# Kernel optimization log

Hardware: AMD Instinct MI355X
Metric: run time of the kernel (lower is better)

Reference implementation:

```python
import jax, jax.numpy as jnp
import numpy as np

B, S, HID = 1, 2048, 2048
H, KVH, D, VD = 32, 8, 128, 128
R = 64  # rope_dim = head_dim * partial_rotary_factor, rounded down to even
N_REP = H // KVH
SCALE = D ** -0.5
NEG = -1e9


def _rotate_half(x):
    half = x.shape[-1] // 2
    return jnp.concatenate([-x[..., half:], x[..., :half]], axis=-1)


def setup_inputs() -> dict:
    key = jax.random.key(0)
    ks = jax.random.split(key, 8)
    hidden_states = jax.random.normal(ks[0], (B, S, HID), dtype=jnp.float32)
    # RoPE angles: standard inverse-frequency positional embedding of width R
    inv_freq = 1.0 / (10000.0 ** (np.arange(0, R, 2, dtype=np.float32) / R))
    pos = np.arange(S, dtype=np.float32)
    freqs = np.outer(pos, inv_freq)                       # [S, R/2]
    emb = np.concatenate([freqs, freqs], axis=-1)         # [S, R]
    cos = jnp.asarray(np.cos(emb))[None].repeat(B, axis=0)  # [B, S, R]
    sin = jnp.asarray(np.sin(emb))[None].repeat(B, axis=0)
    # additive causal mask [B, 1, S, S]
    causal = jnp.triu(jnp.full((S, S), NEG, dtype=jnp.float32), k=1)
    attention_mask = jnp.broadcast_to(causal[None, None], (B, 1, S, S))
    std = 0.02
    Wq = jax.random.normal(ks[1], (H * D, HID), dtype=jnp.float32) * std
    Wk = jax.random.normal(ks[2], (KVH * D, HID), dtype=jnp.float32) * std
    Wv = jax.random.normal(ks[3], (KVH * VD, HID), dtype=jnp.float32) * std
    Wo = jax.random.normal(ks[4], (HID, H * VD), dtype=jnp.float32) * std
    sink_bias = jax.random.normal(ks[5], (H,), dtype=jnp.float32) * 0.5
    return {"hidden_states": hidden_states, "cos": cos, "sin": sin,
            "attention_mask": attention_mask, "Wq": Wq, "Wk": Wk, "Wv": Wv,
            "Wo": Wo, "sink_bias": sink_bias}


def reference(hidden_states, cos, sin, attention_mask, Wq, Wk, Wv, Wo, sink_bias):
    b, s, _ = hidden_states.shape
    # projections -> [B, heads, S, dim]
    q = (hidden_states @ Wq.T).reshape(b, s, H, D).transpose(0, 2, 1, 3)
    k = (hidden_states @ Wk.T).reshape(b, s, KVH, D).transpose(0, 2, 1, 3)
    v = (hidden_states @ Wv.T).reshape(b, s, KVH, VD).transpose(0, 2, 1, 3)
    # partial RoPE on first R dims
    c = cos[:, None, :, :]  # [B,1,S,R]
    si = sin[:, None, :, :]
    q_r, q_n = q[..., :R], q[..., R:]
    k_r, k_n = k[..., :R], k[..., R:]
    q = jnp.concatenate([q_r * c + _rotate_half(q_r) * si, q_n], axis=-1)
    k = jnp.concatenate([k_r * c + _rotate_half(k_r) * si, k_n], axis=-1)
    # GQA: repeat kv heads
    k_rep = jnp.repeat(k, N_REP, axis=1)
    v_rep = jnp.repeat(v, N_REP, axis=1)
    scores = jnp.einsum('bhqd,bhkd->bhqk', q, k_rep) * SCALE + attention_mask
    # extra attention-sink logit column per head
    sinks = jnp.broadcast_to(sink_bias.reshape(1, H, 1, 1), (b, H, s, 1))
    aw = jnp.concatenate([scores, sinks], axis=-1)            # [B,H,S,S+1]
    probs = jax.nn.softmax(aw, axis=-1)[..., :-1]             # drop sink column
    out = jnp.einsum('bhqk,bhkd->bhqd', probs, v_rep)
    out = out.transpose(0, 2, 1, 3).reshape(b, s, H * VD)
    return out @ Wo.T
```

## Files before the change

kernel.cpp:

```cpp
#include <hip/hip_runtime.h>

typedef unsigned short u16;
typedef unsigned int   u32;
typedef __bf16  bf16x8 __attribute__((ext_vector_type(8)));
typedef float   f32x4  __attribute__((ext_vector_type(4)));
typedef u16     u16x4  __attribute__((ext_vector_type(4)));
typedef u16     u16x8  __attribute__((ext_vector_type(8)));

#define S_LEN 2048
#define NH 32
#define NKVH 8
#define HD 128
#define QKVST 6144
#define AOST  4096
#define ATT_SCALE 0.08838834764831845f
#define RESCALE_THR 8.0f

__device__ __forceinline__ u16 f2bf(float f){
  u32 u = __builtin_bit_cast(u32, f);
  u += 0x7FFFu + ((u >> 16) & 1u);
  return (u16)(u >> 16);
}
__device__ __forceinline__ float bf2f(u16 h){
  u32 u = ((u32)h) << 16;
  return __builtin_bit_cast(float, u);
}
__device__ __forceinline__ void gload_lds16(const u16* g, u16* l){
  __builtin_amdgcn_global_load_lds(
      (const __attribute__((address_space(1))) void*)g,
      (__attribute__((address_space(3))) void*)l, 16, 0, 0);
}

__global__ void cvt_kernel(const f32x4* __restrict__ in, u16x4* __restrict__ out, int n4){
  int i = blockIdx.x * 256 + threadIdx.x;
  if (i >= n4) return;
  f32x4 v = in[i];
  u16x4 o;
  o[0] = f2bf(v[0]); o[1] = f2bf(v[1]); o[2] = f2bf(v[2]); o[3] = f2bf(v[3]);
  out[i] = o;
}

template<int OUT_BF16, int ROPE>
__global__ __launch_bounds__(256, 2)
void gemm_bt_kernel(const u16* __restrict__ X, const u16* __restrict__ W,
                    void* __restrict__ Cv, int M, int N, int K,
                    const float* __restrict__ cosv, const float* __restrict__ sinv){
  __shared__ __align__(16) u16 As[2][2][128 * 32];
  __shared__ __align__(16) u16 Bs[2][2][128 * 32];
  const int m0 = blockIdx.y * 128, n0 = blockIdx.x * 128;
  const int tid = threadIdx.x;
  const int wave = tid >> 6, lane = tid & 63;
  const int wm = wave >> 1, wn = wave & 1;
  const int g = lane >> 4, ln = lane & 15;
  const int r0 = tid >> 2;
  const int cc = (tid & 3) * 8;
  f32x4 acc[4][4] = {};
  const u16* xa0 = X + (size_t)(m0 + r0) * K + cc;
  const u16* xa1 = X + (size_t)(m0 + r0 + 64) * K + cc;
  const u16* wb0 = W + (size_t)(n0 + r0) * K + cc;
  const u16* wb1 = W + (size_t)(n0 + r0 + 64) * K + cc;

  auto stage = [&](int buf, int k0){
    #pragma unroll
    for (int s = 0; s < 2; s++){
      const int kc = k0 + s * 32;
      gload_lds16(xa0 + kc, &As[buf][s][tid * 8]);
      gload_lds16(xa1 + kc, &As[buf][s][2048 + tid * 8]);
      gload_lds16(wb0 + kc, &Bs[buf][s][tid * 8]);
      gload_lds16(wb1 + kc, &Bs[buf][s][2048 + tid * 8]);
    }
  };

  stage(0, 0);
  __syncthreads();
  int cur = 0;
  for (int k0 = 0; k0 < K; k0 += 64){
    if (k0 + 64 < K) stage(cur ^ 1, k0 + 64);
    #pragma unroll
    for (int s = 0; s < 2; s++){
      bf16x8 a[4], b[4];
      #pragma unroll
      for (int f = 0; f < 4; f++) a[f] = *(const bf16x8*)&As[cur][s][(wm * 64 + f * 16 + ln) * 32 + g * 8];
      #pragma unroll
      for (int f = 0; f < 4; f++) b[f] = *(const bf16x8*)&Bs[cur][s][(wn * 64 + f * 16 + ln) * 32 + g * 8];
      __builtin_amdgcn_s_setprio(1);
      #pragma unroll
      for (int i = 0; i < 4; i++)
        #pragma unroll
        for (int j = 0; j < 4; j++)
          acc[i][j] = __builtin_amdgcn_mfma_f32_16x16x32_bf16(a[i], b[j], acc[i][j], 0, 0, 0);
      __builtin_amdgcn_s_setprio(0);
    }
    __syncthreads();
    cur ^= 1;
  }
  if (ROPE && wn == 0 && n0 < 5120){
    #pragma unroll
    for (int i = 0; i < 4; i++)
      #pragma unroll
      for (int r = 0; r < 4; r++){
        const int row = m0 + wm * 64 + i * 16 + g * 4 + r;
        #pragma unroll
        for (int j = 0; j < 2; j++){
          const int d = j * 16 + ln;
          float c  = cosv[row * 64 + d];
          float sn = sinv[row * 64 + d];
          float x0 = acc[i][j][r], x1 = acc[i][j + 2][r];
          acc[i][j][r]     = x0 * c - x1 * sn;
          acc[i][j + 2][r] = x1 * c + x0 * sn;
        }
      }
  }
  #pragma unroll
  for (int i = 0; i < 4; i++)
    #pragma unroll
    for (int j = 0; j < 4; j++)
      #pragma unroll
      for (int r = 0; r < 4; r++){
        int row = m0 + wm * 64 + i * 16 + g * 4 + r;
        int col = n0 + wn * 64 + j * 16 + ln;
        if (OUT_BF16) ((u16*)Cv)[(size_t)row * N + col] = f2bf(acc[i][j][r]);
        else          ((float*)Cv)[(size_t)row * N + col] = acc[i][j][r];
      }
}

__global__ void vtrans_kernel(const u16* __restrict__ QKV, u16* __restrict__ VT){
  int idx = blockIdx.x * 256 + threadIdx.x;
  if (idx >= NKVH * HD * S_LEN) return;
  int s   = idx & (S_LEN - 1);
  int vd  = (idx >> 11) & (HD - 1);
  int kvh = idx >> 18;
  VT[idx] = QKV[(size_t)s * QKVST + 5120 + kvh * HD + vd];
}

__global__ __launch_bounds__(256, 2)
void attn_kernel(const u16* __restrict__ QKV, const u16* __restrict__ VT,
                 const float* __restrict__ sinkb, u16* __restrict__ AO){
  __shared__ __align__(16) u16 Ks[2][64 * 128];
  __shared__ __align__(16) u16 Vs[2][144 * 64];
  __shared__ __align__(16) u16 Ps[4][16 * 64];
  const int b   = blockIdx.x;
  const int kvh = b & 7;
  const int h   = kvh * 4 + ((b >> 3) & 3);
  const int qt  = 31 - (b >> 5);
  const int tid = threadIdx.x;
  const int w = tid >> 6, lane = tid & 63;
  const int g = lane >> 4, ln = lane & 15;
  const int q0 = qt * 64;
  const int qw = q0 + w * 16;

  const u16* Kbase = QKV + 4096 + kvh * HD;
  const u16* Vbase = VT + (size_t)kvh * HD * S_LEN;

  auto stage = [&](int buf, int kt){
    const int k0 = kt * 64;
    #pragma unroll
    for (int p = 0; p < 4; p++){
      int idx = p * 256 + tid;
      int r = idx >> 4, c16 = idx & 15;
      gload_lds16(Kbase + (size_t)(k0 + r) * QKVST + ((c16 ^ (r & 7)) * 8), &Ks[buf][idx * 8]);
    }
    #pragma unroll
    for (int p = 0; p < 4; p++){
      int idx = p * 256 + tid;
      int vd = idx >> 3, c8 = idx & 7;
      gload_lds16(Vbase + (size_t)vd * S_LEN + k0 + ((c8 ^ (vd & 7)) * 8), &Vs[buf][idx * 8]);
    }
  };

  for (int i = tid; i < 16 * 64; i += 256){
    u16 v = (i < 64) ? (u16)0x3F80 : (u16)0;
    Vs[0][128 * 64 + i] = v;
    Vs[1][128 * 64 + i] = v;
  }

  bf16x8 qf[4];
  const u16* qrow = QKV + (size_t)(qw + ln) * QKVST + h * HD;
  #pragma unroll
  for (int t = 0; t < 4; t++) qf[t] = *(const bf16x8*)(qrow + t * 32 + g * 8);

  f32x4 O[9] = {};
  float m_r[4];
  #pragma unroll
  for (int r = 0; r < 4; r++) m_r[r] = -3.0e38f;

  const int nkt = qt + 1;
  stage(0, 0);
  __syncthreads();
  int cur = 0;

  for (int kt = 0; kt < nkt; kt++){
    const int k0 = kt * 64;
    if (kt + 1 < nkt) stage(cur ^ 1, kt + 1);

    const u16* Kc = Ks[cur];
    f32x4 sc[4] = {};
    __builtin_amdgcn_s_setprio(1);
    #pragma unroll
    for (int f = 0; f < 4; f++){
      const int krow = f * 16 + ln;
      #pragma unroll
      for (int t = 0; t < 4; t++){
        bf16x8 kf = *(const bf16x8*)&Kc[krow * 128 + ((t * 32 + g * 8) ^ ((ln & 7) << 3))];
        sc[f] = __builtin_amdgcn_mfma_f32_16x16x32_bf16(qf[t], kf, sc[f], 0, 0, 0);
      }
    }
    __builtin_amdgcn_s_setprio(0);

    const bool diag = (kt == qt);
    float pv[4][4];
    #pragma unroll
    for (int f = 0; f < 4; f++)
      #pragma unroll
      for (int r = 0; r < 4; r++){
        float v = sc[f][r] * ATT_SCALE;
        if (diag && (k0 + f * 16 + ln > qw + g * 4 + r)) v = -1e30f;
        pv[f][r] = v;
      }
    float mx[4];
    #pragma unroll
    for (int r = 0; r < 4; r++){
      float t = fmaxf(fmaxf(pv[0][r], pv[1][r]), fmaxf(pv[2][r], pv[3][r]));
      #pragma unroll
      for (int d = 1; d < 16; d <<= 1) t = fmaxf(t, __shfl_xor(t, d));
      mx[r] = t;
    }
    int ok = (mx[0] <= m_r[0] + RESCALE_THR) & (mx[1] <= m_r[1] + RESCALE_THR)
           & (mx[2] <= m_r[2] + RESCALE_THR) & (mx[3] <= m_r[3] + RESCALE_THR);
    if (!__all(ok)){
      float sf_[4];
      #pragma unroll
      for (int r = 0; r < 4; r++){
        float mn = fmaxf(m_r[r], mx[r]);
        sf_[r] = __expf(m_r[r] - mn);
        m_r[r] = mn;
      }
      #pragma unroll
      for (int fn = 0; fn < 9; fn++)
        #pragma unroll
        for (int r = 0; r < 4; r++) O[fn][r] *= sf_[r];
    }
    u16* Pw = Ps[w];
    #pragma unroll
    for (int r = 0; r < 4; r++){
      const int row = g * 4 + r;
      #pragma unroll
      for (int f = 0; f < 4; f++){
        float p = __expf(pv[f][r] - m_r[r]);
        Pw[row * 64 + ((f * 16 + ln) ^ ((row & 7) << 3))] = f2bf(p);
      }
    }
    const u16* Vc = Vs[cur];
    bf16x8 pa0 = *(const bf16x8*)&Pw[ln * 64 + ((g * 8)      ^ ((ln & 7) << 3))];
    bf16x8 pa1 = *(const bf16x8*)&Pw[ln * 64 + ((32 + g * 8) ^ ((ln & 7) << 3))];
    __builtin_amdgcn_s_setprio(1);
    #pragma unroll
    for (int fn = 0; fn < 9; fn++){
      const int vr = fn * 16 + ln;
      bf16x8 v0 = *(const bf16x8*)&Vc[vr * 64 + ((g * 8)      ^ ((ln & 7) << 3))];
      bf16x8 v1 = *(const bf16x8*)&Vc[vr * 64 + ((32 + g * 8) ^ ((ln & 7) << 3))];
      O[fn] = __builtin_amdgcn_mfma_f32_16x16x32_bf16(pa0, v0, O[fn], 0, 0, 0);
      O[fn] = __builtin_amdgcn_mfma_f32_16x16x32_bf16(pa1, v1, O[fn], 0, 0, 0);
    }
    __builtin_amdgcn_s_setprio(0);

    __syncthreads();
    cur ^= 1;
  }
  float sb = sinkb[h];
  #pragma unroll
  for (int r = 0; r < 4; r++){
    float l = __shfl(O[8][r], lane & 48);
    float mt = fmaxf(m_r[r], sb);
    float lt = l * __expf(m_r[r] - mt) + __expf(sb - mt);
    float osc = __expf(m_r[r] - mt) / lt;
    #pragma unroll
    for (int fn = 0; fn < 8; fn++)
      AO[(size_t)(qw + g * 4 + r) * AOST + h * HD + fn * 16 + ln] = f2bf(O[fn][r] * osc);
  }
}

extern "C" void kernel_launch(void* const* d_in, const int* in_sizes, int n_in,
                              void* d_out, int out_size, void* d_ws, size_t ws_size,
                              hipStream_t stream){
  (void)in_sizes; (void)n_in; (void)out_size; (void)ws_size;
  const float* hs    = (const float*)d_in[0];
  const float* cosv  = (const float*)d_in[1];
  const float* sinv  = (const float*)d_in[2];
  const float* Wq    = (const float*)d_in[4];
  const float* Wk    = (const float*)d_in[5];
  const float* Wv    = (const float*)d_in[6];
  const float* Wo    = (const float*)d_in[7];
  const float* sinkb = (const float*)d_in[8];
  float* out = (float*)d_out;

  char* ws = (char*)d_ws;
  u16* XB    = (u16*)(ws);
  u16* WQKVB = (u16*)(ws + 8388608);
  u16* WOB   = (u16*)(ws + 33554432);
  u16* QKV   = (u16*)(ws + 50331648);
  u16* VT    = (u16*)(ws + 75497472);
  u16* AO    = (u16*)(ws + 79691776);

  cvt_kernel<<<4096, 256, 0, stream>>>((const f32x4*)hs, (u16x4*)XB, 1048576);
  cvt_kernel<<<8192, 256, 0, stream>>>((const f32x4*)Wq, (u16x4*)WQKVB, 2097152);
  cvt_kernel<<<2048, 256, 0, stream>>>((const f32x4*)Wk, (u16x4*)(WQKVB + 4096 * 2048), 524288);
  cvt_kernel<<<2048, 256, 0, stream>>>((const f32x4*)Wv, (u16x4*)(WQKVB + 5120 * 2048), 524288);
  cvt_kernel<<<8192, 256, 0, stream>>>((const f32x4*)Wo, (u16x4*)WOB, 2097152);

  gemm_bt_kernel<1, 1><<<dim3(48, 16), 256, 0, stream>>>(XB, WQKVB, QKV, 2048, 6144, 2048, cosv, sinv);

  vtrans_kernel<<<8192, 256, 0, stream>>>(QKV, VT);

  attn_kernel<<<dim3(1024), 256, 0, stream>>>(QKV, VT, sinkb, AO);

  gemm_bt_kernel<0, 0><<<dim3(16, 16), 256, 0, stream>>>(AO, WOB, out, 2048, 2048, 4096, nullptr, nullptr);
}
```

Before: 259.3 us.

## Merge conversion launches, fold softmax scale into Q, skip masked diagonal tiles

The five fp32-to-bf16 conversion launches become one kernel, relying on the workspace buffers being laid out contiguously. The QKV GEMM epilogue pre-multiplies Q by scale*log2e so attention can use exp2 without a per-score multiply. The row sum now comes from a separate MFMA against a ones fragment instead of a padded ninth V tile, which shrinks V shared memory. On the causal diagonal, fully masked 16-column fragments are skipped in QK and set to zero in P. Together these cut launch overhead and some ALU and MFMA work. The trade-offs are Q being rounded to bf16 after scaling and extra branching inside the attention loop.

```diff
diff --git a/kernel.cpp b/kernel.cpp
--- a/kernel.cpp
+++ b/kernel.cpp
@@ -14,7 +14,9 @@
 #define QKVST 6144
 #define AOST  4096
 #define ATT_SCALE 0.08838834764831845f
-#define RESCALE_THR 8.0f
+#define LOG2E 1.4426950408889634f
+#define QSC2 (ATT_SCALE * LOG2E)
+#define RESCALE_THR2 11.5f
 
 __device__ __forceinline__ u16 f2bf(float f){
   u32 u = __builtin_bit_cast(u32, f);
@@ -31,10 +33,17 @@
       (__attribute__((address_space(3))) void*)l, 16, 0, 0);
 }
 
-__global__ void cvt_kernel(const f32x4* __restrict__ in, u16x4* __restrict__ out, int n4){
+__global__ void cvt_all_kernel(const f32x4* __restrict__ hs, const f32x4* __restrict__ wq,
+                               const f32x4* __restrict__ wk, const f32x4* __restrict__ wv,
+                               const f32x4* __restrict__ wo, u16x4* __restrict__ out){
   int i = blockIdx.x * 256 + threadIdx.x;
-  if (i >= n4) return;
-  f32x4 v = in[i];
+  const f32x4* src; int off;
+  if      (i < 1048576){ src = hs; off = i; }
+  else if (i < 3145728){ src = wq; off = i - 1048576; }
+  else if (i < 3670016){ src = wk; off = i - 3145728; }
+  else if (i < 4194304){ src = wv; off = i - 3670016; }
+  else                 { src = wo; off = i - 4194304; }
+  f32x4 v = src[off];
   u16x4 o;
   o[0] = f2bf(v[0]); o[1] = f2bf(v[1]); o[2] = f2bf(v[2]); o[3] = f2bf(v[3]);
   out[i] = o;
@@ -94,22 +103,32 @@
     __syncthreads();
     cur ^= 1;
   }
-  if (ROPE && wn == 0 && n0 < 5120){
-    #pragma unroll
-    for (int i = 0; i < 4; i++)
-      #pragma unroll
-      for (int r = 0; r < 4; r++){
-        const int row = m0 + wm * 64 + i * 16 + g * 4 + r;
-        #pragma unroll
-        for (int j = 0; j < 2; j++){
-          const int d = j * 16 + ln;
-          float c  = cosv[row * 64 + d];
-          float sn = sinv[row * 64 + d];
-          float x0 = acc[i][j][r], x1 = acc[i][j + 2][r];
-          acc[i][j][r]     = x0 * c - x1 * sn;
-          acc[i][j + 2][r] = x1 * c + x0 * sn;
+  if (ROPE){
+    if (wn == 0 && n0 < 5120){
+      #pragma unroll
+      for (int i = 0; i < 4; i++)
+        #pragma unroll
+        for (int r = 0; r < 4; r++){
+          const int row = m0 + wm * 64 + i * 16 + g * 4 + r;
+          #pragma unroll
+          for (int j = 0; j < 2; j++){
+            const int d = j * 16 + ln;
+            float c  = cosv[row * 64 + d];
+            float sn = sinv[row * 64 + d];
+            float x0 = acc[i][j][r], x1 = acc[i][j + 2][r];
+            acc[i][j][r]     = x0 * c - x1 * sn;
+            acc[i][j + 2][r] = x1 * c + x0 * sn;
+          }
         }
-      }
+    }
+    if (n0 < 4096){
+      #pragma unroll
+      for (int i = 0; i < 4; i++)
+        #pragma unroll
+        for (int j = 0; j < 4; j++)
+          #pragma unroll
+          for (int r = 0; r < 4; r++) acc[i][j][r] *= QSC2;
+    }
   }
   #pragma unroll
   for (int i = 0; i < 4; i++)
@@ -137,7 +156,7 @@
 void attn_kernel(const u16* __restrict__ QKV, const u16* __restrict__ VT,
                  const float* __restrict__ sinkb, u16* __restrict__ AO){
   __shared__ __align__(16) u16 Ks[2][64 * 128];
-  __shared__ __align__(16) u16 Vs[2][144 * 64];
+  __shared__ __align__(16) u16 Vs[2][128 * 64];
   __shared__ __align__(16) u16 Ps[4][16 * 64];
   const int b   = blockIdx.x;
   const int kvh = b & 7;
@@ -168,18 +187,18 @@
     }
   };
 
-  for (int i = tid; i < 16 * 64; i += 256){
-    u16 v = (i < 64) ? (u16)0x3F80 : (u16)0;
-    Vs[0][128 * 64 + i] = v;
-    Vs[1][128 * 64 + i] = v;
-  }
+  u16x8 ob;
+  #pragma unroll
+  for (int j = 0; j < 8; j++) ob[j] = (ln == 0) ? (u16)0x3F80 : (u16)0;
+  const bf16x8 onesf = __builtin_bit_cast(bf16x8, ob);
 
   bf16x8 qf[4];
   const u16* qrow = QKV + (size_t)(qw + ln) * QKVST + h * HD;
   #pragma unroll
   for (int t = 0; t < 4; t++) qf[t] = *(const bf16x8*)(qrow + t * 32 + g * 8);
 
-  f32x4 O[9] = {};
+  f32x4 O[8] = {};
+  f32x4 L = {};
   float m_r[4];
   #pragma unroll
   for (int r = 0; r < 4; r++) m_r[r] = -3.0e38f;
@@ -193,52 +212,59 @@
     const int k0 = kt * 64;
     if (kt + 1 < nkt) stage(cur ^ 1, kt + 1);
 
+    const int nf = min(4, ((qw + 15 - k0) >> 4) + 1);
+
     const u16* Kc = Ks[cur];
     f32x4 sc[4] = {};
     __builtin_amdgcn_s_setprio(1);
     #pragma unroll
     for (int f = 0; f < 4; f++){
-      const int krow = f * 16 + ln;
-      #pragma unroll
-      for (int t = 0; t < 4; t++){
-        bf16x8 kf = *(const bf16x8*)&Kc[krow * 128 + ((t * 32 + g * 8) ^ ((ln & 7) << 3))];
-        sc[f] = __builtin_amdgcn_mfma_f32_16x16x32_bf16(qf[t], kf, sc[f], 0, 0, 0);
+      if (f < nf){
+        const int krow = f * 16 + ln;
+        #pragma unroll
+        for (int t = 0; t < 4; t++){
+          bf16x8 kf = *(const bf16x8*)&Kc[krow * 128 + ((t * 32 + g * 8) ^ ((ln & 7) << 3))];
+          sc[f] = __builtin_amdgcn_mfma_f32_16x16x32_bf16(qf[t], kf, sc[f], 0, 0, 0);
+        }
       }
     }
     __builtin_amdgcn_s_setprio(0);
 
-    const bool diag = (kt == qt);
-    float pv[4][4];
-    #pragma unroll
-    for (int f = 0; f < 4; f++)
-      #pragma unroll
-      for (int r = 0; r < 4; r++){
-        float v = sc[f][r] * ATT_SCALE;
-        if (diag && (k0 + f * 16 + ln > qw + g * 4 + r)) v = -1e30f;
-        pv[f][r] = v;
-      }
+    const bool needmask = (k0 + 63 > qw);
+    if (needmask){
+      #pragma unroll
+      for (int f = 0; f < 4; f++)
+        if (f < nf)
+          #pragma unroll
+          for (int r = 0; r < 4; r++)
+            if (k0 + f * 16 + ln > qw + g * 4 + r) sc[f][r] = -1e30f;
+    }
     float mx[4];
     #pragma unroll
     for (int r = 0; r < 4; r++){
-      float t = fmaxf(fmaxf(pv[0][r], pv[1][r]), fmaxf(pv[2][r], pv[3][r]));
+      float t = -1e30f;
+      #pragma unroll
+      for (int f = 0; f < 4; f++) if (f < nf) t = fmaxf(t, sc[f][r]);
       #pragma unroll
       for (int d = 1; d < 16; d <<= 1) t = fmaxf(t, __shfl_xor(t, d));
       mx[r] = t;
     }
-    int ok = (mx[0] <= m_r[0] + RESCALE_THR) & (mx[1] <= m_r[1] + RESCALE_THR)
-           & (mx[2] <= m_r[2] + RESCALE_THR) & (mx[3] <= m_r[3] + RESCALE_THR);
+    int ok = (mx[0] <= m_r[0] + RESCALE_THR2) & (mx[1] <= m_r[1] + RESCALE_THR2)
+           & (mx[2] <= m_r[2] + RESCALE_THR2) & (mx[3] <= m_r[3] + RESCALE_THR2);
     if (!__all(ok)){
       float sf_[4];
       #pragma unroll
       for (int r = 0; r < 4; r++){
         float mn = fmaxf(m_r[r], mx[r]);
-        sf_[r] = __expf(m_r[r] - mn);
+        sf_[r] = exp2f(m_r[r] - mn);
         m_r[r] = mn;
       }
       #pragma unroll
-      for (int fn = 0; fn < 9; fn++)
+      for (int fn = 0; fn < 8; fn++)
         #pragma unroll
         for (int r = 0; r < 4; r++) O[fn][r] *= sf_[r];
+      #pragma unroll
+      for (int r = 0; r < 4; r++) L[r] *= sf_[r];
     }
     u16* Pw = Ps[w];
     #pragma unroll
@@ -246,8 +272,8 @@
       const int row = g * 4 + r;
       #pragma unroll
       for (int f = 0; f < 4; f++){
-        float p = __expf(pv[f][r] - m_r[r]);
-        Pw[row * 64 + ((f * 16 + ln) ^ ((row & 7) << 3))] = f2bf(p);
+        u16 pb = (f < nf) ? f2bf(exp2f(sc[f][r] - m_r[r])) : (u16)0;
+        Pw[row * 64 + ((f * 16 + ln) ^ ((row & 7) << 3))] = pb;
       }
     }
     const u16* Vc = Vs[cur];
@@ -255,25 +281,27 @@
     bf16x8 pa1 = *(const bf16x8*)&Pw[ln * 64 + ((32 + g * 8) ^ ((ln & 7) << 3))];
     __builtin_amdgcn_s_setprio(1);
     #pragma unroll
-    for (int fn = 0; fn < 9; fn++){
+    for (int fn = 0; fn < 8; fn++){
       const int vr = fn * 16 + ln;
       bf16x8 v0 = *(const bf16x8*)&Vc[vr * 64 + ((g * 8)      ^ ((ln & 7) << 3))];
       bf16x8 v1 = *(const bf16x8*)&Vc[vr * 64 + ((32 + g * 8) ^ ((ln & 7) << 3))];
       O[fn] = __builtin_amdgcn_mfma_f32_16x16x32_bf16(pa0, v0, O[fn], 0, 0, 0);
       O[fn] = __builtin_amdgcn_mfma_f32_16x16x32_bf16(pa1, v1, O[fn], 0, 0, 0);
     }
+    L = __builtin_amdgcn_mfma_f32_16x16x32_bf16(pa0, onesf, L, 0, 0, 0);
+    L = __builtin_amdgcn_mfma_f32_16x16x32_bf16(pa1, onesf, L, 0, 0, 0);
     __builtin_amdgcn_s_setprio(0);
 
     __syncthreads();
     cur ^= 1;
   }
-  float sb = sinkb[h];
+  float sb2 = sinkb[h] * LOG2E;
   #pragma unroll
   for (int r = 0; r < 4; r++){
-    float l = __shfl(O[8][r], lane & 48);
-    float mt = fmaxf(m_r[r], sb);
-    float lt = l * __expf(m_r[r] - mt) + __expf(sb - mt);
-    float osc = __expf(m_r[r] - mt) / lt;
+    float l = __shfl(L[r], lane & 48);
+    float mt = fmaxf(m_r[r], sb2);
+    float lt = l * exp2f(m_r[r] - mt) + exp2f(sb2 - mt);
+    float osc = exp2f(m_r[r] - mt) / lt;
     #pragma unroll
     for (int fn = 0; fn < 8; fn++)
       AO[(size_t)(qw + g * 4 + r) * AOST + h * HD + fn * 16 + ln] = f2bf(O[fn][r] * osc);
@@ -302,11 +330,9 @@
   u16* VT    = (u16*)(ws + 75497472);
   u16* AO    = (u16*)(ws + 79691776);
 
-  cvt_kernel<<<4096, 256, 0, stream>>>((const f32x4*)hs, (u16x4*)XB, 1048576);
-  cvt_kernel<<<8192, 256, 0, stream>>>((const f32x4*)Wq, (u16x4*)WQKVB, 2097152);
-  cvt_kernel<<<2048, 256, 0, stream>>>((const f32x4*)Wk, (u16x4*)(WQKVB + 4096 * 2048), 524288);
-  cvt_kernel<<<2048, 256, 0, stream>>>((const f32x4*)Wv, (u16x4*)(WQKVB + 5120 * 2048), 524288);
-  cvt_kernel<<<8192, 256, 0, stream>>>((const f32x4*)Wo, (u16x4*)WOB, 2097152);
+  cvt_all_kernel<<<24576, 256, 0, stream>>>((const f32x4*)hs, (const f32x4*)Wq,
+                                            (const f32x4*)Wk, (const f32x4*)Wv,
+                                            (const f32x4*)Wo, (u16x4*)ws);
 
   gemm_bt_kernel<1, 1><<<dim3(48, 16), 256, 0, stream>>>(XB, WQKVB, QKV, 2048, 6144, 2048, cosv, sinv);
 
```

New measurement: 269.2 us. +3.8%, slower.
